# Kernel optimization log

Hardware: AMD Instinct MI355X
Metric: run time of the kernel (lower is better)

## Reference

```python
import jax, jax.numpy as jnp
import numpy as np

B, S, D, P, H = 32, 1024, 512, 720, 4   # batch, seq_len (=codebook_size), enc_in, pred_len, heads
COMMIT_W, ORTHO_W = 1.0, 0.8


def setup_inputs() -> dict:
    key = jax.random.key(0)
    ks = jax.random.split(key, 6)
    return {
        "x": jax.random.normal(ks[0], (B, S, D), jnp.float32),
        "w_in": jax.random.normal(ks[1], (H * D, D), jnp.float32) * 0.02,   # project_in: dim -> heads*dim
        "b_in": jnp.zeros((H * D,), jnp.float32),
        "embed": jax.random.normal(ks[2], (H, S, D), jnp.float32),          # per-head codebook [h, C, d]
        "w_out": jax.random.normal(ks[3], (D, H * D), jnp.float32) * 0.02,  # project_out: heads*dim -> dim
        "b_out": jnp.zeros((D,), jnp.float32),
        "w_lin": jax.random.normal(ks[4], (P, S), jnp.float32) * 0.02,      # Linear over time axis
        "b_lin": jnp.zeros((P,), jnp.float32),
    }


def reference(x, w_in, b_in, embed, w_out, b_out, w_lin, b_lin):
    C = embed.shape[1]
    # Normalization: subtract last timestep (detached)
    seq_last = jax.lax.stop_gradient(x[:, -1:, :])          # [B,1,D]
    x0 = x - seq_last                                       # [B,S,D]

    # --- VectorQuantize ---
    xi = x0 @ w_in.T + b_in                                 # [B,S,H*D] project_in
    # 'b n (h d) -> h (b n) d' (separate codebook per head)
    f = xi.reshape(B, S, H, D).transpose(2, 0, 1, 3).reshape(H, B * S, D)
    # squared-euclidean distances to codes: [H, B*S, C]
    d2 = (jnp.sum(f * f, -1, keepdims=True)
          - 2.0 * jnp.einsum('hnd,hcd->hnc', f, embed)
          + jnp.sum(embed * embed, -1)[:, None, :])
    ind = jnp.argmin(d2, axis=-1)                           # [H, B*S]
    q = jnp.take_along_axis(embed, ind[:, :, None], axis=1)  # gather -> [H, B*S, D]

    # commitment loss (learnable codebook => quantize NOT detached)
    commit_loss = jnp.mean((q - f) ** 2)
    # orthogonal regularization on full codebook
    normed = embed / jnp.linalg.norm(embed, axis=-1, keepdims=True)
    cs = jnp.einsum('hid,hjd->hij', normed, normed)         # [H,C,C]
    ortho_loss = jnp.sum(cs ** 2) / (H * C * C) - 1.0 / C
    loss = COMMIT_W * commit_loss + ORTHO_W * ortho_loss

    # straight-through estimator
    q_st = f + jax.lax.stop_gradient(q - f)
    # 'h (b n) d -> b n (h d)'
    qo = q_st.reshape(H, B, S, D).transpose(1, 2, 0, 3).reshape(B, S, H * D)
    quantized = qo @ w_out.T + b_out                        # [B,S,D] project_out

    # Linear over the time axis: permute(0,2,1) -> Linear(S->P) -> permute back
    y = jnp.einsum('bnd,pn->bpd', quantized, w_lin) + b_lin[None, :, None]
    y = y + seq_last                                        # [B,P,D]

    indices = ind.reshape(H, B, S).transpose(1, 2, 0)       # [B,S,H]
    return y, indices, loss
```

## Files before the change

kernel.cpp:

```cpp
#include <hip/hip_runtime.h>
#include <stdint.h>

typedef unsigned int u32;
typedef unsigned long long u64;
typedef _Float16 f16;
typedef __attribute__((ext_vector_type(8))) _Float16 f16x8;
typedef __attribute__((ext_vector_type(4))) _Float16 f16x4;
typedef __attribute__((ext_vector_type(2))) _Float16 f16x2;
typedef __attribute__((ext_vector_type(4))) float f32x4;

#define MFMA16(a, b, c) __builtin_amdgcn_mfma_f32_16x16x32_f16((a), (b), (c), 0, 0, 0)
#define MARGIN 2.0f
#define WAITV(n) asm volatile("s_waitcnt vmcnt(" #n ")" ::: "memory")

__device__ __forceinline__ u32 ford(float x) { u32 u = __float_as_uint(x); return (u & 0x80000000u) ? ~u : (u | 0x80000000u); }
__device__ __forceinline__ float iford(u32 v) { u32 u = (v & 0x80000000u) ? (v & 0x7FFFFFFFu) : ~v; return __uint_as_float(u); }
__device__ __forceinline__ int xswz(int i, int n) { return (i & 7) * (n >> 3) + (i >> 3); }

typedef __attribute__((address_space(1))) const unsigned char ga_t;
typedef __attribute__((address_space(3))) unsigned char la_t;
__device__ __forceinline__ void gl16(const void* g, void* l) {
  __builtin_amdgcn_global_load_lds((ga_t*)g, (la_t*)l, 16, 0, 0);
}

template <int LDK>
__device__ __forceinline__ void stg8k(const f16* gRowBase, int ktile, char* sdst, int tid) {
#pragma unroll
  for (int it = 0; it < 2; ++it) {
    const int u = (tid + (it << 8)) << 4;
    const int r = u >> 6, s = (u >> 4) & 3;
    const char* src = (const char*)gRowBase + (size_t)r * (LDK * 2) + ((size_t)ktile << 6) +
                      (size_t)((s ^ ((r >> 1) & 3)) << 4);
    gl16(src, sdst + u);
  }
}

template <int MODE>
__global__ __launch_bounds__(256, (MODE == 0 || MODE == 3) ? 2 : 3) void gemm2(
    const f16* __restrict__ Ah, const f16* __restrict__ Al,
    const f16* __restrict__ Bh, const f16* __restrict__ Bl,
    int chrows,
    void* __restrict__ out0, void* __restrict__ out1,
    const float* __restrict__ bias, const float* __restrict__ aux,
    u64* __restrict__ slots) {
  constexpr bool K1 = (MODE == 0);
  constexpr bool SC = (MODE == 3);
  constexpr int LDK = (MODE == 2 || MODE == 4) ? 1024 : 512;
  constexpr int D = K1 ? 2 : 3;
  constexpr int KT = (MODE == 2 || MODE == 4) ? 32 : 16;
  constexpr int MT = SC ? 8 : 4;
  constexpr int BUF = K1 ? 32768 : (SC ? 24576 : 16384);
  constexpr int LDS_SZ = D * BUF + (SC ? 1024 : 0);
  __shared__ char lds[LDS_SZ];

  const int tid = threadIdx.x;
  const int lane = tid & 63, wid = tid >> 6;
  const int wm = wid >> 1, wn = wid & 1;

  int blkm, blkn, z = 0;
  {
    const int s = xswz(blockIdx.x, gridDim.x);
    if constexpr (MODE == 0) { blkn = s & 15; blkm = s >> 4; }
    else if constexpr (MODE == 1) { blkn = s & 3; blkm = s >> 2; z = blkm >> 3; }
    else if constexpr (MODE == 2) { blkn = s & 3; blkm = (s >> 2) & 3; z = s >> 4; }
    else if constexpr (MODE == 3) {
      const int bph = (chrows >> 8) << 3;
      z = s / bph;
      const int rem = s - z * bph;
      blkm = rem >> 3; blkn = rem & 7;
    } else { const int r2 = s % 24; blkm = r2 % 6; blkn = r2 / 6; z = s / 24; }
  }

  int* cntL = (int*)(lds + D * BUF);
  if constexpr (SC) cntL[tid] = 0;

  const f16 *Ab, *Bb, *Alb = nullptr, *Blb = nullptr;
  if constexpr (MODE == 0) {
    Ab = Ah + (size_t)blkm * 65536;
    Alb = Al + (size_t)blkm * 65536;
    Bb = Bh + (size_t)blkn * 65536;
    Blb = Bl + (size_t)blkn * 65536;
  } else if constexpr (MODE == 1) {
    Ab = Ah + (size_t)blkm * 65536;
    Bb = Bh + (size_t)z * 262144 + (size_t)blkn * 65536;
  } else if constexpr (MODE == 2) {
    Ab = Ah + (size_t)z * 524288 + (size_t)blkm * 131072;
    Bb = Bh + (size_t)z * 524288 + (size_t)blkn * 131072;
  } else if constexpr (MODE == 3) {
    Ab = Ah + ((size_t)z * chrows + (size_t)blkm * 256) * 512;
    Bb = Bh + (size_t)z * 524288 + (size_t)blkn * 65536;
  } else {
    Ab = Ah + (size_t)blkm * 131072;
    Bb = Bh + (size_t)z * 524288 + (size_t)blkn * 131072;
  }

  f32x4 acc[MT][4];
#pragma unroll
  for (int i = 0; i < MT; ++i)
#pragma unroll
    for (int j = 0; j < 4; ++j) acc[i][j] = f32x4{0.f, 0.f, 0.f, 0.f};

  auto stage = [&](int kt, char* nb) {
    stg8k<LDK>(Ab, kt, nb, tid);
    if constexpr (SC) stg8k<LDK>(Ab + 65536, kt, nb + 8192, tid);
    if constexpr (K1) stg8k<LDK>(Alb, kt, nb + 8192, tid);
    stg8k<LDK>(Bb, kt, nb + 16384 - (SC || K1 ? 0 : 8192), tid);
    if constexpr (K1) stg8k<LDK>(Blb, kt, nb + 24576, tid);
  };

#pragma unroll
  for (int d = 0; d < D - 1; ++d) stage(d, lds + d * BUF);

#pragma unroll
  for (int kc = 0; kc < KT; ++kc) {
    if (kc + D - 1 < KT) stage(kc + D - 1, lds + ((kc + D - 1) % D) * BUF);
    const int nf = KT - 1 - kc;
    if constexpr (SC) {
      if (nf >= 2) WAITV(12);
      else if (nf == 1) WAITV(6);
      else WAITV(0);
    } else if constexpr (K1) {
      if (nf >= 1) WAITV(8);
      else WAITV(0);
    } else {
      if (nf >= 2) WAITV(8);
      else if (nf == 1) WAITV(4);
      else WAITV(0);
    }
    __builtin_amdgcn_s_barrier();
    const char* cbuf = lds + (kc % D) * BUF;
    f16x8 ah[MT], al[4];
#pragma unroll
    for (int mt = 0; mt < MT; ++mt) {
      const int rr = wm * (MT * 16) + mt * 16 + (lane & 15);
      const int o = rr * 64 + (((lane >> 4) ^ ((rr >> 1) & 3)) << 4);
      ah[mt] = *(const f16x8*)(cbuf + o);
      if constexpr (K1) al[mt] = *(const f16x8*)(cbuf + 8192 + o);
    }
    __builtin_amdgcn_s_setprio(1);
#pragma unroll
    for (int nt = 0; nt < 4; ++nt) {
      const int rn = wn * 64 + nt * 16 + (lane & 15);
      const int o = rn * 64 + (((lane >> 4) ^ ((rn >> 1) & 3)) << 4);
      const f16x8 bh = *(const f16x8*)(cbuf + (K1 || SC ? 16384 : 8192) + o);
      f16x8 bl;
      if constexpr (K1) bl = *(const f16x8*)(cbuf + 24576 + o);
#pragma unroll
      for (int mt = 0; mt < MT; ++mt) {
        if constexpr (K1) {
          acc[mt][nt] = MFMA16(al[mt], bh, acc[mt][nt]);
          acc[mt][nt] = MFMA16(ah[mt], bl, acc[mt][nt]);
        }
        acc[mt][nt] = MFMA16(ah[mt], bh, acc[mt][nt]);
      }
    }
    __builtin_amdgcn_s_setprio(0);
    __builtin_amdgcn_s_barrier();
  }

  if constexpr (MODE == 0) {
    f16* fh = (f16*)out0;
    f16* fl = (f16*)out1;
#pragma unroll
    for (int nt = 0; nt < 4; ++nt) {
      const int gc = blkn * 128 + wn * 64 + nt * 16 + (lane & 15);
      const float bv = bias[gc];
      const int h = gc >> 9, d = gc & 511;
#pragma unroll
      for (int mt = 0; mt < 4; ++mt)
#pragma unroll
        for (int r = 0; r < 4; ++r) {
          const int grow = blkm * 128 + wm * 64 + mt * 16 + ((lane >> 4) << 2) + r;
          const float v = acc[mt][nt][r] * 6.103515625e-05f + bv;
          const f16 hv = (f16)v;
          const size_t off = ((size_t)h * chrows + grow) * 512 + d;
          fh[off] = hv;
          fl[off] = (f16)(v - (float)hv);
        }
    }
  } else if constexpr (MODE == 1) {
    f16* o = (f16*)out0;
#pragma unroll
    for (int nt = 0; nt < 4; ++nt) {
      const int gc = blkn * 128 + wn * 64 + nt * 16 + (lane & 15);
#pragma unroll
      for (int mt = 0; mt < 4; ++mt)
#pragma unroll
        for (int r = 0; r < 4; ++r) {
          const size_t grow = (size_t)blkm * 128 + wm * 64 + mt * 16 + ((lane >> 4) << 2) + r;
          o[grow * 512 + gc] = (f16)acc[mt][nt][r];
        }
    }
  } else if constexpr (MODE == 2) {
    float ssum = 0.f;
#pragma unroll
    for (int mt = 0; mt < 4; ++mt)
#pragma unroll
      for (int nt = 0; nt < 4; ++nt)
#pragma unroll
        for (int r = 0; r < 4; ++r) ssum += acc[mt][nt][r] * acc[mt][nt][r];
#pragma unroll
    for (int o = 1; o < 64; o <<= 1) ssum += __shfl_xor(ssum, o);
    float* wp = (float*)lds;
    __syncthreads();
    if (lane == 0) wp[wid] = ssum;
    __syncthreads();
    if (tid == 0) {
      const float p = wp[0] + wp[1] + wp[2] + wp[3];
      atomicAdd(slots + (blockIdx.x & 63), (u64)llrintf(p * 16777216.f));
    }
  } else if constexpr (MODE == 3) {
    u64* candG = (u64*)out0;
    const int h = z;
    float escol[4];
    int cc[4];
#pragma unroll
    for (int nt = 0; nt < 4; ++nt) {
      cc[nt] = blkn * 128 + wn * 64 + nt * 16 + (lane & 15);
      escol[nt] = aux[h * 1024 + cc[nt]];
    }
#pragma unroll
    for (int mt = 0; mt < 8; ++mt)
#pragma unroll
      for (int r = 0; r < 4; ++r) {
        const int row_l = wm * 128 + mt * 16 + ((lane >> 4) << 2) + r;
        float vals[4];
        float mn = 3.4e38f;
#pragma unroll
        for (int nt = 0; nt < 4; ++nt) {
          const float v = escol[nt] - 2.0f * acc[mt][nt][r];
          vals[nt] = v;
          mn = fminf(mn, v);
        }
#pragma unroll
        for (int o = 1; o < 16; o <<= 1) mn = fminf(mn, __shfl_xor(mn, o));
        const float lim = mn + MARGIN;
#pragma unroll
        for (int nt = 0; nt < 4; ++nt)
          if (vals[nt] <= lim) {
            const int p = atomicAdd(&cntL[row_l], 1);
            if (p < 8) {
              const size_t grow = (size_t)blkm * 256 + row_l;
              candG[(((size_t)h * chrows + grow) * 8 + blkn) * 8 + p] =
                  ((u64)ford(vals[nt]) << 32) | (u32)cc[nt];
            }
          }
      }
  } else {
    float* oy = (float*)out0 + (size_t)z * 368640;
    const float* xseq = aux + (size_t)z * 524288 + 523776;
    float sl[4];
    int gd[4];
#pragma unroll
    for (int nt = 0; nt < 4; ++nt) {
      gd[nt] = blkn * 128 + wn * 64 + nt * 16 + (lane & 15);
      sl[nt] = xseq[gd[nt]];
    }
#pragma unroll
    for (int mt = 0; mt < 4; ++mt)
#pragma unroll
      for (int r = 0; r < 4; ++r) {
        const int p = blkm * 128 + wm * 64 + mt * 16 + ((lane >> 4) << 2) + r;
        if (p < 720) {
          const float bp = bias[p];
#pragma unroll
          for (int nt = 0; nt < 4; ++nt) oy[(size_t)p * 512 + gd[nt]] = acc[mt][nt][r] + bp + sl[nt];
        }
      }
  }
}

__global__ __launch_bounds__(256, 4) void rescore_k(
    const u64* __restrict__ candG, const f16* __restrict__ fh,
    const f16* __restrict__ fl, const float* __restrict__ embed,
    int n0, int shCH,
    int* __restrict__ indw, float* __restrict__ indout, u64* __restrict__ cslots) {
  const int tid = threadIdx.x, lane = tid & 63, wid = tid >> 6;
  const int r = blockIdx.x * 4 + wid;
  const int h = r >> shCH, row = r & ((1 << shCH) - 1);
  u64 cu = candG[(size_t)r * 64 + lane];
  u64 mn = cu;
#pragma unroll
  for (int o = 1; o < 64; o <<= 1) { const u64 t = __shfl_xor(mn, o); if (t < mn) mn = t; }
  const float lim = iford((u32)(mn >> 32)) + MARGIN;
  const bool pass = iford((u32)(cu >> 32)) <= lim;
  u64 mask = __ballot(pass);
  float fv[8];
  {
    const size_t fo = (size_t)r * 512 + lane * 8;
    const f16x8 hv = *(const f16x8*)(fh + fo);
    const f16x8 lv = *(const f16x8*)(fl + fo);
#pragma unroll
    for (int j = 0; j < 8; ++j) fv[j] = (float)hv[j] + (float)lv[j];
  }
  double bestd = 1e300;
  int bestc = 0x7FFFFFFF;
  while (mask) {
    const int src = __ffsll((unsigned long long)mask) - 1;
    mask &= mask - 1;
    const int c = (int)(u32)__shfl(cu, src);
    const float* e = embed + ((size_t)h * 1024 + c) * 512 + lane * 8;
    const float4 e0 = *(const float4*)e, e1 = *(const float4*)(e + 4);
    const float ev[8] = {e0.x, e0.y, e0.z, e0.w, e1.x, e1.y, e1.z, e1.w};
    double sd = 0.0;
#pragma unroll
    for (int j = 0; j < 8; ++j) { const double d = (double)fv[j] - (double)ev[j]; sd += d * d; }
#pragma unroll
    for (int o = 1; o < 64; o <<= 1) sd += __shfl_xor(sd, o);
    if (sd < bestd || (sd == bestd && c < bestc)) { bestd = sd; bestc = c; }
  }
  if (lane == 0) {
    const int n = n0 + row;
    indw[(size_t)n * 4 + h] = bestc;
    indout[(size_t)n * 4 + h] = (float)bestc;
    atomicAdd(cslots + (blockIdx.x & 255), (u64)llrint(bestd * 65536.0));
  }
}

__global__ __launch_bounds__(256) void quantize_qT(
    const int* __restrict__ indw, const f16* __restrict__ Ep,
    const float* __restrict__ b_out, f16* __restrict__ qT) {
  const int tid = threadIdx.x;
  const int b = blockIdx.x >> 4, s0 = (blockIdx.x & 15) << 6;
  __shared__ int inds[64][4];
  inds[tid >> 2][tid & 3] = indw[(size_t)(b * 1024 + s0 + (tid >> 2)) * 4 + (tid & 3)];
  __syncthreads();
  const int d0 = tid * 2;
  const float ba0 = b_out[d0], ba1 = b_out[d0 + 1];
  u32 r0[32], r1[32];
  f16 t0 = (f16)0.f, t1 = (f16)0.f;
#pragma unroll
  for (int ss = 0; ss < 64; ++ss) {
    float a0 = ba0, a1 = ba1;
#pragma unroll
    for (int h = 0; h < 4; ++h) {
      const int c = inds[ss][h];
      const f16x2 p = *(const f16x2*)(Ep + (((size_t)h * 1024 + c) * 512 + d0));
      a0 += (float)p[0];
      a1 += (float)p[1];
    }
    const f16 q0 = (f16)a0, q1 = (f16)a1;
    if (ss & 1) {
      f16x2 w0; w0[0] = t0; w0[1] = q0; __builtin_memcpy(&r0[ss >> 1], &w0, 4);
      f16x2 w1; w1[0] = t1; w1[1] = q1; __builtin_memcpy(&r1[ss >> 1], &w1, 4);
    } else { t0 = q0; t1 = q1; }
  }
  const size_t o0 = ((size_t)b * 512 + d0) * 1024 + s0;
#pragma unroll
  for (int i = 0; i < 8; ++i) {
    uint4 v; v.x = r0[4 * i]; v.y = r0[4 * i + 1]; v.z = r0[4 * i + 2]; v.w = r0[4 * i + 3];
    *(uint4*)(qT + o0 + (size_t)i * 8) = v;
  }
  const size_t o1 = o0 + 1024;
#pragma unroll
  for (int i = 0; i < 8; ++i) {
    uint4 v; v.x = r1[4 * i]; v.y = r1[4 * i + 1]; v.z = r1[4 * i + 2]; v.w = r1[4 * i + 3];
    *(uint4*)(qT + o1 + (size_t)i * 8) = v;
  }
}

__global__ __launch_bounds__(256) void prep_x0(const float* __restrict__ x, int n0,
                                               f16* __restrict__ ht, f16* __restrict__ lt) {
  const int id = blockIdx.x * 256 + threadIdx.x;
  const int k8 = id & 63, r = id >> 6;
  const int n = n0 + r, b = n >> 10;
  const float* ap = x + (size_t)n * 512 + k8 * 8;
  const float* sp = x + (size_t)b * 524288 + 523776 + k8 * 8;
  const float4 a0 = *(const float4*)ap, a1 = *(const float4*)(ap + 4);
  const float4 s0 = *(const float4*)sp, s1 = *(const float4*)(sp + 4);
  const float v[8] = {(a0.x - s0.x) * 16.f, (a0.y - s0.y) * 16.f, (a0.z - s0.z) * 16.f,
                      (a0.w - s0.w) * 16.f, (a1.x - s1.x) * 16.f, (a1.y - s1.y) * 16.f,
                      (a1.z - s1.z) * 16.f, (a1.w - s1.w) * 16.f};
  f16x8 hv, lv;
#pragma unroll
  for (int j = 0; j < 8; ++j) { const f16 h = (f16)v[j]; hv[j] = h; lv[j] = (f16)(v[j] - (float)h); }
  const size_t off = (size_t)r * 512 + k8 * 8;
  *(f16x8*)(ht + off) = hv;
  *(f16x8*)(lt + off) = lv;
}

__global__ __launch_bounds__(256) void prep_win(const float* __restrict__ src,
                                                f16* __restrict__ hi, f16* __restrict__ lo) {
  const size_t e = ((size_t)blockIdx.x * 256 + threadIdx.x) * 4;
  const float4 v = *(const float4*)(src + e);
  const float w[4] = {v.x * 1024.f, v.y * 1024.f, v.z * 1024.f, v.w * 1024.f};
  f16x4 hv, lv;
#pragma unroll
  for (int j = 0; j < 4; ++j) { const f16 h = (f16)w[j]; hv[j] = h; lv[j] = (f16)(w[j] - (float)h); }
  *(f16x4*)(hi + e) = hv;
  *(f16x4*)(lo + e) = lv;
}

__global__ __launch_bounds__(256) void prep_embed_k(const float* __restrict__ em,
                                                    f16* __restrict__ ef,
                                                    float* __restrict__ esq,
                                                    float* __restrict__ invn) {
  const int tid = threadIdx.x, lane = tid & 63, wid = tid >> 6;
  const int row = blockIdx.x * 4 + wid;
  const float* er = em + (size_t)row * 512 + lane * 8;
  const float4 a = *(const float4*)er, b = *(const float4*)(er + 4);
  f16x8 v;
  v[0] = (f16)a.x; v[1] = (f16)a.y; v[2] = (f16)a.z; v[3] = (f16)a.w;
  v[4] = (f16)b.x; v[5] = (f16)b.y; v[6] = (f16)b.z; v[7] = (f16)b.w;
  *(f16x8*)(ef + (size_t)row * 512 + lane * 8) = v;
  float s = a.x * a.x + a.y * a.y + a.z * a.z + a.w * a.w +
            b.x * b.x + b.y * b.y + b.z * b.z + b.w * b.w;
#pragma unroll
  for (int o = 1; o < 64; o <<= 1) s += __shfl_xor(s, o);
  if (lane == 0) { esq[row] = s; invn[row] = 1.0f / sqrtf(s); }
}

__global__ __launch_bounds__(256) void prep_wout(const float* __restrict__ src,
                                                 f16* __restrict__ dst) {
  const int id = blockIdx.x * 256 + threadIdx.x;
  const int k8 = id & 63, rg = id >> 6;
  const int d = rg & 511, h = rg >> 9;
  const float* ap = src + (size_t)d * 2048 + h * 512 + k8 * 8;
  const float4 a0 = *(const float4*)ap, a1 = *(const float4*)(ap + 4);
  f16x8 v;
  v[0] = (f16)a0.x; v[1] = (f16)a0.y; v[2] = (f16)a0.z; v[3] = (f16)a0.w;
  v[4] = (f16)a1.x; v[5] = (f16)a1.y; v[6] = (f16)a1.z; v[7] = (f16)a1.w;
  *(f16x8*)(dst + (size_t)h * 262144 + (size_t)d * 512 + k8 * 8) = v;
}

__global__ __launch_bounds__(256) void prep_wlin(const float* __restrict__ src,
                                                 f16* __restrict__ dst) {
  const int id = blockIdx.x * 256 + threadIdx.x;
  const int k8 = id & 127, row = id >> 7;
  float4 a0 = {0.f, 0.f, 0.f, 0.f}, a1 = a0;
  if (row < 720) {
    const float* ap = src + (size_t)row * 1024 + k8 * 8;
    a0 = *(const float4*)ap;
    a1 = *(const float4*)(ap + 4);
  }
  f16x8 v;
  v[0] = (f16)a0.x; v[1] = (f16)a0.y; v[2] = (f16)a0.z; v[3] = (f16)a0.w;
  v[4] = (f16)a1.x; v[5] = (f16)a1.y; v[6] = (f16)a1.z; v[7] = (f16)a1.w;
  *(f16x8*)(dst + (size_t)row * 1024 + k8 * 8) = v;
}

__global__ __launch_bounds__(256) void prep_normT(const float* __restrict__ em,
                                                  const float* __restrict__ invn,
                                                  f16* __restrict__ nT) {
  __shared__ float t[64 * 65];
  const int tid = threadIdx.x;
  const int bx = blockIdx.x;
  const int h = bx >> 7, rem = bx & 127, cb = rem >> 3, db = rem & 7;
  const int c0 = cb * 64, d0 = db * 64;
  const int j = tid & 63, i0 = tid >> 6;
#pragma unroll
  for (int p = 0; p < 16; ++p) {
    const int i = p * 4 + i0;
    t[i * 65 + j] = em[(size_t)h * 524288 + (size_t)(c0 + i) * 512 + d0 + j] * invn[h * 1024 + c0 + i];
  }
  __syncthreads();
#pragma unroll
  for (int p = 0; p < 16; ++p) {
    const int i = p * 4 + i0;
    nT[(size_t)h * 524288 + (size_t)(d0 + i) * 1024 + c0 + j] = (f16)t[j * 65 + i];
  }
}

__global__ void finalize_k(const u64* __restrict__ cs, const u64* __restrict__ gs,
                           float* __restrict__ out) {
  const int lane = threadIdx.x;
  u64 c = cs[lane] + cs[lane + 64] + cs[lane + 128] + cs[lane + 192];
  u64 g = gs[lane];
#pragma unroll
  for (int o = 1; o < 64; o <<= 1) {
    c += __shfl_xor(c, o);
    g += __shfl_xor(g, o);
  }
  if (lane == 0) {
    const double commit = (double)c / 65536.0 / 67108864.0;
    const double ortho = (double)g / 16777216.0 / 4194304.0 - (1.0 / 1024.0);
    out[11927552] = (float)(commit + 0.8 * ortho);
  }
}

__global__ void ws_fail_k(float* out) {
  if (threadIdx.x == 0) out[11927552] = -777777.0f;
}

extern "C" void kernel_launch(void* const* d_in, const int* in_sizes, int n_in,
                              void* d_out, int out_size, void* d_ws, size_t ws_size,
                              hipStream_t stream) {
  (void)in_sizes; (void)n_in; (void)out_size;
  const float* x = (const float*)d_in[0];
  const float* w_in = (const float*)d_in[1];
  const float* b_in = (const float*)d_in[2];
  const float* embed = (const float*)d_in[3];
  const float* w_out = (const float*)d_in[4];
  const float* b_out = (const float*)d_in[5];
  const float* w_lin = (const float*)d_in[6];
  const float* b_lin = (const float*)d_in[7];
  float* out = (float*)d_out;
  char* ws = (char*)d_ws;

  constexpr size_t SZ_WIN = 2097152, SZ_EFT = 4194304, SZ_WOUT = 2097152;
  constexpr size_t SZ_EP = 4194304, SZ_WLIN = 1572864, SZ_NT = 4194304;
  constexpr size_t SZ_SMALL = 16384 + 16384 + 524288 + 2048 + 512;
  constexpr size_t FIXED = SZ_WIN * 2 + SZ_EFT + SZ_WOUT + SZ_EP + SZ_WLIN + SZ_NT + SZ_SMALL;

  int CH = 16384, shCH = 14;
  if (ws_size < FIXED + (size_t)16384 * 12288) { CH = 8192; shCH = 13; }
  if (ws_size < FIXED + (size_t)CH * 12288) {
    ws_fail_k<<<1, 64, 0, stream>>>(out);
    return;
  }

  size_t off = 0;
  f16* x0h = (f16*)(ws + off); off += (size_t)CH * 1024;
  f16* x0l = (f16*)(ws + off); off += (size_t)CH * 1024;
  f16* fh = (f16*)(ws + off); off += (size_t)CH * 4096;
  f16* fl = (f16*)(ws + off); off += (size_t)CH * 4096;
  u64* cand = (u64*)(ws + off); off += (size_t)CH * 2048;
  f16* winh = (f16*)(ws + off); off += SZ_WIN;
  f16* winl = (f16*)(ws + off); off += SZ_WIN;
  f16* eft = (f16*)(ws + off); off += SZ_EFT;
  f16* wout = (f16*)(ws + off); off += SZ_WOUT;
  f16* Ep = (f16*)(ws + off); off += SZ_EP;
  f16* wlint = (f16*)(ws + off); off += SZ_WLIN;
  f16* nT = (f16*)(ws + off); off += SZ_NT;
  float* esq = (float*)(ws + off); off += 16384;
  float* invn = (float*)(ws + off); off += 16384;
  int* indw = (int*)(ws + off); off += 524288;
  u64* cslots = (u64*)(ws + off); off += 2048;
  u64* gslots = (u64*)(ws + off); off += 512;
  f16* qT = (f16*)ws;

  hipMemsetAsync((void*)cslots, 0, 2560, stream);

  prep_win<<<1024, 256, 0, stream>>>(w_in, winh, winl);
  prep_embed_k<<<1024, 256, 0, stream>>>(embed, eft, esq, invn);
  prep_normT<<<512, 256, 0, stream>>>(embed, invn, nT);
  prep_wout<<<512, 256, 0, stream>>>(w_out, wout);
  prep_wlin<<<384, 256, 0, stream>>>(w_lin, wlint);

  gemm2<1><<<128, 256, 0, stream>>>(eft, nullptr, wout, nullptr, 0,
                                    Ep, nullptr, nullptr, nullptr, nullptr);
  gemm2<2><<<64, 256, 0, stream>>>(nT, nullptr, nT, nullptr, 0,
                                   nullptr, nullptr, nullptr, nullptr, gslots);

  for (int c0 = 0; c0 < 32768; c0 += CH) {
    prep_x0<<<CH / 4, 256, 0, stream>>>(x, c0, x0h, x0l);
    gemm2<0><<<(CH / 128) * 16, 256, 0, stream>>>(x0h, x0l, winh, winl, CH,
                                                  fh, fl, b_in, nullptr, nullptr);
    hipMemsetAsync((void*)cand, 0xFF, (size_t)CH * 2048, stream);
    gemm2<3><<<(CH / 256) * 32, 256, 0, stream>>>(fh, nullptr, eft, nullptr, CH,
                                                  cand, nullptr, nullptr, esq, nullptr);
    rescore_k<<<CH, 256, 0, stream>>>(cand, fh, fl, embed, c0, shCH,
                                      indw, out + 11796480, cslots);
  }

  quantize_qT<<<512, 256, 0, stream>>>(indw, Ep, b_out, qT);
  gemm2<4><<<768, 256, 0, stream>>>(wlint, nullptr, qT, nullptr, 0,
                                    out, nullptr, b_lin, x, nullptr);
  finalize_k<<<1, 64, 0, stream>>>(cslots, gslots, out);
}
```

Measured before the change: 698.7 us.

## Add 8-wave 512-thread GEMM kernel with 128B K-tiles for projection and scoring

```diff
diff --git a/kernel.cpp b/kernel.cpp
--- a/kernel.cpp
+++ b/kernel.cpp
@@ -23,6 +23,274 @@
   __builtin_amdgcn_global_load_lds((ga_t*)g, (la_t*)l, 16, 0, 0);
 }
 
+__device__ __forceinline__ void stgp(const f16* g, int kt, char* sdst, int tid) {
+#pragma unroll
+  for (int it = 0; it < 2; ++it) {
+    const int u = (tid + (it << 9)) << 4;
+    const int r = u >> 7, sl = (u >> 4) & 7;
+    const char* src = (const char*)g + (size_t)r * 1024 + ((size_t)kt << 7) +
+                      (size_t)((sl ^ (r & 7)) << 4);
+    gl16(src, sdst + u);
+  }
+}
+
+__device__ __forceinline__ f16x8 rdf(const char* bb, int pb, int rr, int ks, int lane) {
+  return *(const f16x8*)(bb + pb + rr * 128 +
+                         ((((ks << 2) + (lane >> 4)) ^ (rr & 7)) << 4));
+}
+
+template <bool ISK1>
+__global__ __launch_bounds__(512, 1) void gemm8(
+    const f16* __restrict__ A0, const f16* __restrict__ A1,
+    const f16* __restrict__ B0, const f16* __restrict__ B1,
+    int chrows, void* __restrict__ out0, void* __restrict__ out1,
+    const float* __restrict__ bias, const float* __restrict__ aux) {
+  __shared__ char lds[131072 + (ISK1 ? 0 : 4096)];
+  const int tid = threadIdx.x;
+  const int lane = tid & 63, wid = tid >> 6;
+  const int wm = wid >> 2, wn = wid & 3;
+
+  int blkm, blkn, z = 0;
+  {
+    const int s = xswz(blockIdx.x, gridDim.x);
+    if constexpr (ISK1) { blkn = s & 15; blkm = s >> 4; }
+    else {
+      const int bph = (chrows >> 8) << 2;
+      z = s / bph;
+      const int rem = s - z * bph;
+      blkm = rem >> 2; blkn = rem & 3;
+    }
+  }
+
+  if constexpr (!ISK1) {
+    ((int*)(lds + 131072))[tid] = 0;
+    ((int*)(lds + 131072))[tid + 512] = 0;
+  }
+
+  const f16 *p0, *p1, *p2, *p3;
+  if constexpr (ISK1) {
+    p0 = A0 + (size_t)blkm * 65536;
+    p1 = A1 + (size_t)blkm * 65536;
+    p2 = B0 + (size_t)blkn * 65536;
+    p3 = B1 + (size_t)blkn * 65536;
+  } else {
+    p0 = A0 + ((size_t)z * chrows + (size_t)blkm * 256) * 512;
+    p1 = p0 + 65536;
+    p2 = B0 + (size_t)z * 524288 + (size_t)blkn * 131072;
+    p3 = p2 + 65536;
+  }
+
+  constexpr int NACC = ISK1 ? 8 : 32;
+  f32x4 acc[NACC];
+#pragma unroll
+  for (int i = 0; i < NACC; ++i) acc[i] = f32x4{0.f, 0.f, 0.f, 0.f};
+
+  stgp(p0, 0, lds + 0, tid);
+  stgp(p1, 0, lds + 16384, tid);
+  stgp(p2, 0, lds + 32768, tid);
+  stgp(p3, 0, lds + 49152, tid);
+
+#pragma unroll
+  for (int kc = 0; kc < 8; ++kc) {
+    const char* bb = lds + (kc & 1) * 65536;
+    char* nb = lds + ((kc + 1) & 1) * 65536;
+    const bool pf = (kc + 1 < 8);
+    WAITV(0);
+    __builtin_amdgcn_s_barrier();
+
+    if constexpr (!ISK1) {
+      f16x8 a[4][2], b[4][2];
+      const int pbA = wm * 16384;
+      const int pbB = 32768 + (wn >> 1) * 16384;
+      const int rB = (wn & 1) * 64 + (lane & 15);
+#pragma unroll
+      for (int mt = 0; mt < 4; ++mt)
+#pragma unroll
+        for (int ks = 0; ks < 2; ++ks) a[mt][ks] = rdf(bb, pbA, mt * 16 + (lane & 15), ks, lane);
+#pragma unroll
+      for (int nt = 0; nt < 2; ++nt)
+#pragma unroll
+        for (int ks = 0; ks < 2; ++ks) b[nt][ks] = rdf(bb, pbB, rB + nt * 16, ks, lane);
+      if (pf) stgp(p0, kc + 1, nb + 0, tid);
+      __builtin_amdgcn_s_setprio(1);
+#pragma unroll
+      for (int nt = 0; nt < 2; ++nt)
+#pragma unroll
+        for (int mt = 0; mt < 4; ++mt)
+#pragma unroll
+          for (int ks = 0; ks < 2; ++ks) acc[mt * 4 + nt] = MFMA16(a[mt][ks], b[nt][ks], acc[mt * 4 + nt]);
+      __builtin_amdgcn_s_setprio(0);
+#pragma unroll
+      for (int nt = 2; nt < 4; ++nt)
+#pragma unroll
+        for (int ks = 0; ks < 2; ++ks) b[nt][ks] = rdf(bb, pbB, rB + nt * 16, ks, lane);
+      if (pf) stgp(p1, kc + 1, nb + 16384, tid);
+      __builtin_amdgcn_s_setprio(1);
+#pragma unroll
+      for (int nt = 2; nt < 4; ++nt)
+#pragma unroll
+        for (int mt = 0; mt < 4; ++mt)
+#pragma unroll
+          for (int ks = 0; ks < 2; ++ks) acc[mt * 4 + nt] = MFMA16(a[mt][ks], b[nt][ks], acc[mt * 4 + nt]);
+      __builtin_amdgcn_s_setprio(0);
+#pragma unroll
+      for (int mt = 0; mt < 4; ++mt)
+#pragma unroll
+        for (int ks = 0; ks < 2; ++ks) a[mt][ks] = rdf(bb, pbA, (mt + 4) * 16 + (lane & 15), ks, lane);
+      if (pf) stgp(p2, kc + 1, nb + 32768, tid);
+      __builtin_amdgcn_s_setprio(1);
+#pragma unroll
+      for (int nt = 2; nt < 4; ++nt)
+#pragma unroll
+        for (int mt = 0; mt < 4; ++mt)
+#pragma unroll
+          for (int ks = 0; ks < 2; ++ks) acc[(mt + 4) * 4 + nt] = MFMA16(a[mt][ks], b[nt][ks], acc[(mt + 4) * 4 + nt]);
+      __builtin_amdgcn_s_setprio(0);
+      if (pf) stgp(p3, kc + 1, nb + 49152, tid);
+      __builtin_amdgcn_s_setprio(1);
+#pragma unroll
+      for (int nt = 0; nt < 2; ++nt)
+#pragma unroll
+        for (int mt = 0; mt < 4; ++mt)
+#pragma unroll
+          for (int ks = 0; ks < 2; ++ks) acc[(mt + 4) * 4 + nt] = MFMA16(a[mt][ks], b[nt][ks], acc[(mt + 4) * 4 + nt]);
+      __builtin_amdgcn_s_setprio(0);
+    } else {
+      f16x8 ah[2][2], al[2][2], bh[2][2], bl[2][2];
+      const int rA = wm * 64 + (lane & 15);
+      const int rB = wn * 32 + (lane & 15);
+#pragma unroll
+      for (int mt = 0; mt < 2; ++mt)
+#pragma unroll
+        for (int ks = 0; ks < 2; ++ks) {
+          ah[mt][ks] = rdf(bb, 0, rA + mt * 16, ks, lane);
+          al[mt][ks] = rdf(bb, 16384, rA + mt * 16, ks, lane);
+        }
+#pragma unroll
+      for (int ks = 0; ks < 2; ++ks) {
+        bh[0][ks] = rdf(bb, 32768, rB, ks, lane);
+        bl[0][ks] = rdf(bb, 49152, rB, ks, lane);
+      }
+      if (pf) stgp(p0, kc + 1, nb + 0, tid);
+      __builtin_amdgcn_s_setprio(1);
+#pragma unroll
+      for (int mt = 0; mt < 2; ++mt)
+#pragma unroll
+        for (int ks = 0; ks < 2; ++ks) {
+          acc[mt * 2] = MFMA16(al[mt][ks], bh[0][ks], acc[mt * 2]);
+          acc[mt * 2] = MFMA16(ah[mt][ks], bl[0][ks], acc[mt * 2]);
+          acc[mt * 2] = MFMA16(ah[mt][ks], bh[0][ks], acc[mt * 2]);
+        }
+      __builtin_amdgcn_s_setprio(0);
+#pragma unroll
+      for (int ks = 0; ks < 2; ++ks) {
+        bh[1][ks] = rdf(bb, 32768, rB + 16, ks, lane);
+        bl[1][ks] = rdf(bb, 49152, rB + 16, ks, lane);
+      }
+      if (pf) stgp(p1, kc + 1, nb + 16384, tid);
+      __builtin_amdgcn_s_setprio(1);
+#pragma unroll
+      for (int mt = 0; mt < 2; ++mt)
+#pragma unroll
+        for (int ks = 0; ks < 2; ++ks) {
+          acc[mt * 2 + 1] = MFMA16(al[mt][ks], bh[1][ks], acc[mt * 2 + 1]);
+          acc[mt * 2 + 1] = MFMA16(ah[mt][ks], bl[1][ks], acc[mt * 2 + 1]);
+          acc[mt * 2 + 1] = MFMA16(ah[mt][ks], bh[1][ks], acc[mt * 2 + 1]);
+        }
+      __builtin_amdgcn_s_setprio(0);
+#pragma unroll
+      for (int mt = 0; mt < 2; ++mt)
+#pragma unroll
+        for (int ks = 0; ks < 2; ++ks) {
+          ah[mt][ks] = rdf(bb, 0, rA + (mt + 2) * 16, ks, lane);
+          al[mt][ks] = rdf(bb, 16384, rA + (mt + 2) * 16, ks, lane);
+        }
+      if (pf) stgp(p2, kc + 1, nb + 32768, tid);
+      __builtin_amdgcn_s_setprio(1);
+#pragma unroll
+      for (int mt = 0; mt < 2; ++mt)
+#pragma unroll
+        for (int ks = 0; ks < 2; ++ks) {
+          acc[(mt + 2) * 2 + 1] = MFMA16(al[mt][ks], bh[1][ks], acc[(mt + 2) * 2 + 1]);
+          acc[(mt + 2) * 2 + 1] = MFMA16(ah[mt][ks], bl[1][ks], acc[(mt + 2) * 2 + 1]);
+          acc[(mt + 2) * 2 + 1] = MFMA16(ah[mt][ks], bh[1][ks], acc[(mt + 2) * 2 + 1]);
+        }
+      __builtin_amdgcn_s_setprio(0);
+      if (pf) stgp(p3, kc + 1, nb + 49152, tid);
+      __builtin_amdgcn_s_setprio(1);
+#pragma unroll
+      for (int mt = 0; mt < 2; ++mt)
+#pragma unroll
+        for (int ks = 0; ks < 2; ++ks) {
+          acc[(mt + 2) * 2] = MFMA16(al[mt][ks], bh[0][ks], acc[(mt + 2) * 2]);
+          acc[(mt + 2) * 2] = MFMA16(ah[mt][ks], bl[0][ks], acc[(mt + 2) * 2]);
+          acc[(mt + 2) * 2] = MFMA16(ah[mt][ks], bh[0][ks], acc[(mt + 2) * 2]);
+        }
+      __builtin_amdgcn_s_setprio(0);
+    }
+  }
+
+  if constexpr (ISK1) {
+    f16* fh = (f16*)out0;
+    f16* fl = (f16*)out1;
+#pragma unroll
+    for (int nt = 0; nt < 2; ++nt) {
+      const int gc = blkn * 128 + wn * 32 + nt * 16 + (lane & 15);
+      const float bv = bias[gc];
+      const int h = gc >> 9, d = gc & 511;
+#pragma unroll
+      for (int mt = 0; mt < 4; ++mt)
+#pragma unroll
+        for (int r = 0; r < 4; ++r) {
+          const int grow = blkm * 128 + wm * 64 + mt * 16 + ((lane >> 4) << 2) + r;
+          const float v = acc[mt * 2 + nt][r] * 6.103515625e-05f + bv;
+          const f16 hv = (f16)v;
+          const size_t off = ((size_t)h * chrows + grow) * 512 + d;
+          fh[off] = hv;
+          fl[off] = (f16)(v - (float)hv);
+        }
+    }
+  } else {
+    int* cntL = (int*)(lds + 131072);
+    u64* candG = (u64*)out0;
+    const int h = z;
+    float escol[4];
+    int cc[4];
+#pragma unroll
+    for (int nt = 0; nt < 4; ++nt) {
+      cc[nt] = blkn * 256 + wn * 64 + nt * 16 + (lane & 15);
+      escol[nt] = aux[h * 1024 + cc[nt]];
+    }
+#pragma unroll
+    for (int mt = 0; mt < 8; ++mt)
+#pragma unroll
+      for (int r = 0; r < 4; ++r) {
+        const int row_l = wm * 128 + mt * 16 + ((lane >> 4) << 2) + r;
+        float vals[4];
+        float mn = 3.4e38f;
+#pragma unroll
+        for (int nt = 0; nt < 4; ++nt) {
+          const float v = escol[nt] - 2.0f * acc[mt * 4 + nt][r];
+          vals[nt] = v;
+          mn = fminf(mn, v);
+        }
+#pragma unroll
+        for (int o = 1; o < 16; o <<= 1) mn = fminf(mn, __shfl_xor(mn, o));
+        const float lim = mn + MARGIN;
+#pragma unroll
+        for (int nt = 0; nt < 4; ++nt)
+          if (vals[nt] <= lim) {
+            const int p = atomicAdd(&cntL[row_l * 4 + wn], 1);
+            if (p < 4) {
+              const size_t grow = (size_t)blkm * 256 + row_l;
+              candG[((size_t)h * chrows + grow) * 64 + blkn * 16 + wn * 4 + p] =
+                  ((u64)ford(vals[nt]) << 32) | (u32)cc[nt];
+            }
+          }
+      }
+  }
+}
+
 template <int LDK>
 __device__ __forceinline__ void stg8k(const f16* gRowBase, int ktile, char* sdst, int tid) {
 #pragma unroll
@@ -36,22 +304,15 @@
 }
 
 template <int MODE>
-__global__ __launch_bounds__(256, (MODE == 0 || MODE == 3) ? 2 : 3) void gemm2(
-    const f16* __restrict__ Ah, const f16* __restrict__ Al,
-    const f16* __restrict__ Bh, const f16* __restrict__ Bl,
-    int chrows,
-    void* __restrict__ out0, void* __restrict__ out1,
-    const float* __restrict__ bias, const float* __restrict__ aux,
-    u64* __restrict__ slots) {
-  constexpr bool K1 = (MODE == 0);
-  constexpr bool SC = (MODE == 3);
+__global__ __launch_bounds__(256, 3) void gemm2(
+    const f16* __restrict__ Ah, const f16* __restrict__ Bh,
+    void* __restrict__ out0, const float* __restrict__ bias,
+    const float* __restrict__ aux, u64* __restrict__ slots) {
   constexpr int LDK = (MODE == 2 || MODE == 4) ? 1024 : 512;
-  constexpr int D = K1 ? 2 : 3;
+  constexpr int D = 3;
   constexpr int KT = (MODE == 2 || MODE == 4) ? 32 : 16;
-  constexpr int MT = SC ? 8 : 4;
-  constexpr int BUF = K1 ? 32768 : (SC ? 24576 : 16384);
-  constexpr int LDS_SZ = D * BUF + (SC ? 1024 : 0);
-  __shared__ char lds[LDS_SZ];
+  constexpr int BUF = 16384;
+  __shared__ char lds[D * BUF];
 
   const int tid = threadIdx.x;
   const int lane = tid & 63, wid = tid >> 6;
@@ -60,54 +321,33 @@
   int blkm, blkn, z = 0;
   {
     const int s = xswz(blockIdx.x, gridDim.x);
-    if constexpr (MODE == 0) { blkn = s & 15; blkm = s >> 4; }
-    else if constexpr (MODE == 1) { blkn = s & 3; blkm = s >> 2; z = blkm >> 3; }
+    if constexpr (MODE == 1) { blkn = s & 3; blkm = s >> 2; z = blkm >> 3; }
     else if constexpr (MODE == 2) { blkn = s & 3; blkm = (s >> 2) & 3; z = s >> 4; }
-    else if constexpr (MODE == 3) {
-      const int bph = (chrows >> 8) << 3;
-      z = s / bph;
-      const int rem = s - z * bph;
-      blkm = rem >> 3; blkn = rem & 7;
-    } else { const int r2 = s % 24; blkm = r2 % 6; blkn = r2 / 6; z = s / 24; }
-  }
-
-  int* cntL = (int*)(lds + D * BUF);
-  if constexpr (SC) cntL[tid] = 0;
-
-  const f16 *Ab, *Bb, *Alb = nullptr, *Blb = nullptr;
-  if constexpr (MODE == 0) {
-    Ab = Ah + (size_t)blkm * 65536;
-    Alb = Al + (size_t)blkm * 65536;
-    Bb = Bh + (size_t)blkn * 65536;
-    Blb = Bl + (size_t)blkn * 65536;
-  } else if constexpr (MODE == 1) {
+    else { const int r2 = s % 24; blkm = r2 % 6; blkn = r2 / 6; z = s / 24; }
+  }
+
+  const f16 *Ab, *Bb;
+  if constexpr (MODE == 1) {
     Ab = Ah + (size_t)blkm * 65536;
     Bb = Bh + (size_t)z * 262144 + (size_t)blkn * 65536;
   } else if constexpr (MODE == 2) {
     Ab = Ah + (size_t)z * 524288 + (size_t)blkm * 131072;
     Bb = Bh + (size_t)z * 524288 + (size_t)blkn * 131072;
-  } else if constexpr (MODE == 3) {
-    Ab = Ah + ((size_t)z * chrows + (size_t)blkm * 256) * 512;
-    Bb = Bh + (size_t)z * 524288 + (size_t)blkn * 65536;
   } else {
     Ab = Ah + (size_t)blkm * 131072;
     Bb = Bh + (size_t)z * 524288 + (size_t)blkn * 131072;
   }
 
-  f32x4 acc[MT][4];
-#pragma unroll
-  for (int i = 0; i < MT; ++i)
+  f32x4 acc[4][4];
+#pragma unroll
+  for (int i = 0; i < 4; ++i)
 #pragma unroll
     for (int j = 0; j < 4; ++j) acc[i][j] = f32x4{0.f, 0.f, 0.f, 0.f};
 
   auto stage = [&](int kt, char* nb) {
     stg8k<LDK>(Ab, kt, nb, tid);
-    if constexpr (SC) stg8k<LDK>(Ab + 65536, kt, nb + 8192, tid);
-    if constexpr (K1) stg8k<LDK>(Alb, kt, nb + 8192, tid);
-    stg8k<LDK>(Bb, kt, nb + 16384 - (SC || K1 ? 0 : 8192), tid);
-    if constexpr (K1) stg8k<LDK>(Blb, kt, nb + 24576, tid);
+    stg8k<LDK>(Bb, kt, nb + 8192, tid);
   };
-
 #pragma unroll
   for (int d = 0; d < D - 1; ++d) stage(d, lds + d * BUF);
 
@@ -115,70 +355,30 @@
   for (int kc = 0; kc < KT; ++kc) {
     if (kc + D - 1 < KT) stage(kc + D - 1, lds + ((kc + D - 1) % D) * BUF);
     const int nf = KT - 1 - kc;
-    if constexpr (SC) {
-      if (nf >= 2) WAITV(12);
-      else if (nf == 1) WAITV(6);
-      else WAITV(0);
-    } else if constexpr (K1) {
-      if (nf >= 1) WAITV(8);
-      else WAITV(0);
-    } else {
-      if (nf >= 2) WAITV(8);
-      else if (nf == 1) WAITV(4);
-      else WAITV(0);
-    }
+    if (nf >= 2) WAITV(8);
+    else if (nf == 1) WAITV(4);
+    else WAITV(0);
     __builtin_amdgcn_s_barrier();
     const char* cbuf = lds + (kc % D) * BUF;
-    f16x8 ah[MT], al[4];
-#pragma unroll
-    for (int mt = 0; mt < MT; ++mt) {
-      const int rr = wm * (MT * 16) + mt * 16 + (lane & 15);
-      const int o = rr * 64 + (((lane >> 4) ^ ((rr >> 1) & 3)) << 4);
-      ah[mt] = *(const f16x8*)(cbuf + o);
-      if constexpr (K1) al[mt] = *(const f16x8*)(cbuf + 8192 + o);
+    f16x8 ah[4];
+#pragma unroll
+    for (int mt = 0; mt < 4; ++mt) {
+      const int rr = wm * 64 + mt * 16 + (lane & 15);
+      ah[mt] = *(const f16x8*)(cbuf + rr * 64 + (((lane >> 4) ^ ((rr >> 1) & 3)) << 4));
     }
     __builtin_amdgcn_s_setprio(1);
 #pragma unroll
     for (int nt = 0; nt < 4; ++nt) {
       const int rn = wn * 64 + nt * 16 + (lane & 15);
-      const int o = rn * 64 + (((lane >> 4) ^ ((rn >> 1) & 3)) << 4);
-      const f16x8 bh = *(const f16x8*)(cbuf + (K1 || SC ? 16384 : 8192) + o);
-      f16x8 bl;
-      if constexpr (K1) bl = *(const f16x8*)(cbuf + 24576 + o);
-#pragma unroll
-      for (int mt = 0; mt < MT; ++mt) {
-        if constexpr (K1) {
-          acc[mt][nt] = MFMA16(al[mt], bh, acc[mt][nt]);
-          acc[mt][nt] = MFMA16(ah[mt], bl, acc[mt][nt]);
-        }
-        acc[mt][nt] = MFMA16(ah[mt], bh, acc[mt][nt]);
-      }
+      const f16x8 bh = *(const f16x8*)(cbuf + 8192 + rn * 64 + (((lane >> 4) ^ ((rn >> 1) & 3)) << 4));
+#pragma unroll
+      for (int mt = 0; mt < 4; ++mt) acc[mt][nt] = MFMA16(ah[mt], bh, acc[mt][nt]);
     }
     __builtin_amdgcn_s_setprio(0);
     __builtin_amdgcn_s_barrier();
   }
 
-  if constexpr (MODE == 0) {
-    f16* fh = (f16*)out0;
-    f16* fl = (f16*)out1;
-#pragma unroll
-    for (int nt = 0; nt < 4; ++nt) {
-      const int gc = blkn * 128 + wn * 64 + nt * 16 + (lane & 15);
-      const float bv = bias[gc];
-      const int h = gc >> 9, d = gc & 511;
-#pragma unroll
-      for (int mt = 0; mt < 4; ++mt)
-#pragma unroll
-        for (int r = 0; r < 4; ++r) {
-          const int grow = blkm * 128 + wm * 64 + mt * 16 + ((lane >> 4) << 2) + r;
-          const float v = acc[mt][nt][r] * 6.103515625e-05f + bv;
-          const f16 hv = (f16)v;
-          const size_t off = ((size_t)h * chrows + grow) * 512 + d;
-          fh[off] = hv;
-          fl[off] = (f16)(v - (float)hv);
-        }
-    }
-  } else if constexpr (MODE == 1) {
+  if constexpr (MODE == 1) {
     f16* o = (f16*)out0;
 #pragma unroll
     for (int nt = 0; nt < 4; ++nt) {
@@ -209,43 +409,6 @@
       const float p = wp[0] + wp[1] + wp[2] + wp[3];
       atomicAdd(slots + (blockIdx.x & 63), (u64)llrintf(p * 16777216.f));
     }
-  } else if constexpr (MODE == 3) {
-    u64* candG = (u64*)out0;
-    const int h = z;
-    float escol[4];
-    int cc[4];
-#pragma unroll
-    for (int nt = 0; nt < 4; ++nt) {
-      cc[nt] = blkn * 128 + wn * 64 + nt * 16 + (lane & 15);
-      escol[nt] = aux[h * 1024 + cc[nt]];
-    }
-#pragma unroll
-    for (int mt = 0; mt < 8; ++mt)
-#pragma unroll
-      for (int r = 0; r < 4; ++r) {
-        const int row_l = wm * 128 + mt * 16 + ((lane >> 4) << 2) + r;
-        float vals[4];
-        float mn = 3.4e38f;
-#pragma unroll
-        for (int nt = 0; nt < 4; ++nt) {
-          const float v = escol[nt] - 2.0f * acc[mt][nt][r];
-          vals[nt] = v;
-          mn = fminf(mn, v);
-        }
-#pragma unroll
-        for (int o = 1; o < 16; o <<= 1) mn = fminf(mn, __shfl_xor(mn, o));
-        const float lim = mn + MARGIN;
-#pragma unroll
-        for (int nt = 0; nt < 4; ++nt)
-          if (vals[nt] <= lim) {
-            const int p = atomicAdd(&cntL[row_l], 1);
-            if (p < 8) {
-              const size_t grow = (size_t)blkm * 256 + row_l;
-              candG[(((size_t)h * chrows + grow) * 8 + blkn) * 8 + p] =
-                  ((u64)ford(vals[nt]) << 32) | (u32)cc[nt];
-            }
-          }
-      }
   } else {
     float* oy = (float*)out0 + (size_t)z * 368640;
     const float* xseq = aux + (size_t)z * 524288 + 523776;
@@ -537,24 +700,21 @@
   prep_wout<<<512, 256, 0, stream>>>(w_out, wout);
   prep_wlin<<<384, 256, 0, stream>>>(w_lin, wlint);
 
-  gemm2<1><<<128, 256, 0, stream>>>(eft, nullptr, wout, nullptr, 0,
-                                    Ep, nullptr, nullptr, nullptr, nullptr);
-  gemm2<2><<<64, 256, 0, stream>>>(nT, nullptr, nT, nullptr, 0,
-                                   nullptr, nullptr, nullptr, nullptr, gslots);
+  gemm2<1><<<128, 256, 0, stream>>>(eft, wout, Ep, nullptr, nullptr, nullptr);
+  gemm2<2><<<64, 256, 0, stream>>>(nT, nT, nullptr, nullptr, nullptr, gslots);
 
   for (int c0 = 0; c0 < 32768; c0 += CH) {
     prep_x0<<<CH / 4, 256, 0, stream>>>(x, c0, x0h, x0l);
-    gemm2<0><<<(CH / 128) * 16, 256, 0, stream>>>(x0h, x0l, winh, winl, CH,
-                                                  fh, fl, b_in, nullptr, nullptr);
+    gemm8<true><<<(CH / 128) * 16, 512, 0, stream>>>(x0h, x0l, winh, winl, CH,
+                                                     fh, fl, b_in, nullptr);
     hipMemsetAsync((void*)cand, 0xFF, (size_t)CH * 2048, stream);
-    gemm2<3><<<(CH / 256) * 32, 256, 0, stream>>>(fh, nullptr, eft, nullptr, CH,
-                                                  cand, nullptr, nullptr, esq, nullptr);
+    gemm8<false><<<(CH / 256) * 16, 512, 0, stream>>>(fh, nullptr, eft, nullptr, CH,
+                                                      cand, nullptr, nullptr, esq);
     rescore_k<<<CH, 256, 0, stream>>>(cand, fh, fl, embed, c0, shCH,
                                       indw, out + 11796480, cslots);
   }
 
   quantize_qT<<<512, 256, 0, stream>>>(indw, Ep, b_out, qT);
-  gemm2<4><<<768, 256, 0, stream>>>(wlint, nullptr, qT, nullptr, 0,
-                                    out, nullptr, b_lin, x, nullptr);
+  gemm2<4><<<768, 256, 0, stream>>>(wlint, qT, out, b_lin, x, nullptr);
   finalize_k<<<1, 64, 0, stream>>>(cslots, gslots, out);
 }
```

After: 697.5 us. Within noise of the previous version (-0.2%).
